# Kernel tuning notes

Measured on AMD Instinct MI355X. Metric: run time of the kernel, lower is better.

The kernel has to match this reference:

```python
import jax, jax.numpy as jnp
import numpy as np

EPS = 1e-5
NEG_SLOPE = 0.01  # F.leaky_relu default

N0, N1, N2 = 100000, 25000, 5000
E0, E1 = 800000, 160000
D_IN, D_HID, D_OUT = 256, 256, 128


def setup_inputs() -> dict:
    key = jax.random.key(0)
    ks = jax.random.split(key, 16)
    inp = {
        "x": jax.random.normal(ks[0], (N0, D_IN), dtype=jnp.float32),
        "src0": jax.random.randint(ks[1], (E0,), 0, N0, dtype=jnp.int32),
        "dst0": jax.random.randint(ks[2], (E0,), 0, N1, dtype=jnp.int32),
        "val0": jnp.arange(E0, dtype=jnp.int32),
        "src1": jax.random.randint(ks[3], (E1,), 0, N1, dtype=jnp.int32),
        "dst1": jax.random.randint(ks[4], (E1,), 0, N2, dtype=jnp.int32),
        "val1": jnp.arange(E1, dtype=jnp.int32),
        "timestamps": jax.random.randint(ks[5], (E0 + E1,), 0, 100, dtype=jnp.int32),
        "time": 50,
        "interval": 10,
        # SAGEConv layer 1 (in -> hidden): lin_l (bias) on aggregated, lin_r (no bias) on root
        "W1l": jax.random.normal(ks[6], (D_IN, D_HID), dtype=jnp.float32) / np.sqrt(D_IN),
        "W1r": jax.random.normal(ks[7], (D_IN, D_HID), dtype=jnp.float32) / np.sqrt(D_IN),
        "b1": jnp.zeros((D_HID,), dtype=jnp.float32),
        # BatchNorm1d params (eval mode: running stats)
        "g1": jnp.ones((D_HID,), dtype=jnp.float32),
        "bt1": jnp.zeros((D_HID,), dtype=jnp.float32),
        "rm1": jax.random.normal(ks[8], (D_HID,), dtype=jnp.float32) * 0.1,
        "rv1": jax.random.uniform(ks[9], (D_HID,), dtype=jnp.float32) + 0.5,
        # SAGEConv layer 2 (hidden -> out)
        "W2l": jax.random.normal(ks[10], (D_HID, D_OUT), dtype=jnp.float32) / np.sqrt(D_HID),
        "W2r": jax.random.normal(ks[11], (D_HID, D_OUT), dtype=jnp.float32) / np.sqrt(D_HID),
        "b2": jnp.zeros((D_OUT,), dtype=jnp.float32),
    }
    return inp


def _time_mask(val, timestamps, time, interval):
    # time_sparse keeps edges whose timestamp is in {time, ..., time+interval-1}
    ts = timestamps[val]
    return (ts >= time) & (ts < time + interval)


def _sage_conv(x_src, x_tgt, src, dst, mask, Wl, Wr, b, n_tgt):
    m = mask.astype(x_src.dtype)
    msg = x_src[src] * m[:, None]               # [E, D] gather + mask
    agg = jax.ops.segment_sum(msg, dst, num_segments=n_tgt)
    deg = jax.ops.segment_sum(m, dst, num_segments=n_tgt)
    agg = agg / jnp.maximum(deg, 1.0)[:, None]  # mean aggregation
    return agg @ Wl + b + x_tgt @ Wr


def reference(x, src0, dst0, val0, src1, dst1, val1, timestamps, time, interval,
              W1l, W1r, b1, g1, bt1, rm1, rv1, W2l, W2r, b2):
    # layer 0: N0 -> N1
    mask0 = _time_mask(val0, timestamps, time, interval)
    h = _sage_conv(x, x[:N1], src0, dst0, mask0, W1l, W1r, b1, N1)
    # BatchNorm1d (eval) + leaky_relu; dropout is identity in eval
    h = (h - rm1) * jax.lax.rsqrt(rv1 + EPS) * g1 + bt1
    h = jnp.where(h >= 0, h, NEG_SLOPE * h)
    # layer 1: N1 -> N2
    mask1 = _time_mask(val1, timestamps, time, interval)
    out = _sage_conv(h, h[:N2], src1, dst1, mask1, W2l, W2r, b2, N2)
    return out, mask1
```

## Files before the change

kernel.cpp:

```cpp
#include <hip/hip_runtime.h>

#define N1c 25000
#define N2c 5000
#define Dc 256
#define DOUTc 128
#define EPSc 1e-5f
#define NEGc 0.01f
#define CAPc 32

typedef __attribute__((ext_vector_type(8))) short short8;
typedef __attribute__((ext_vector_type(4))) float f32x4;

__device__ __forceinline__ ushort f2bf(float f) {
    unsigned u = __float_as_uint(f);
    u += 0x7fffu + ((u >> 16) & 1u);
    return (ushort)(u >> 16);
}
__device__ __forceinline__ float bf2f(ushort u) {
    return __uint_as_float(((unsigned)u) << 16);
}
__device__ __forceinline__ int imin(int a, int b) { return a < b ? a : b; }
__device__ __forceinline__ int imax(int a, int b) { return a > b ? a : b; }

__global__ __launch_bounds__(256) void prep_fill(
    const int* __restrict__ src0, const int* __restrict__ dst0, const int* __restrict__ val0,
    const int* __restrict__ src1, const int* __restrict__ dst1, const int* __restrict__ val1,
    const int* __restrict__ ts, const int* __restrict__ time_p, const int* __restrict__ itv_p,
    const float* __restrict__ W1l, const float* __restrict__ W1r,
    const float* __restrict__ W2l, const float* __restrict__ W2r,
    int E0, int E1,
    ushort* __restrict__ Bt1, ushort* __restrict__ Bt2,
    int* __restrict__ cnt0, int* __restrict__ cnt1,
    int* __restrict__ eidx0, int* __restrict__ eidx1,
    float* __restrict__ mask_out) {
    const int flat = blockIdx.x * blockDim.x + threadIdx.x;
    const int NT = gridDim.x * blockDim.x;
    const int t0 = *time_p, iv = *itv_p;

    for (int i = flat; i < 256 * 512; i += NT) {
        int n = i >> 9, k = i & 511;
        float v = (k < 256) ? W1l[(size_t)k * 256 + n] : W1r[(size_t)(k - 256) * 256 + n];
        Bt1[i] = f2bf(v);
    }
    for (int i = flat; i < 128 * 512; i += NT) {
        int n = i >> 9, k = i & 511;
        float v = (k < 256) ? W2l[(size_t)k * 128 + n] : W2r[(size_t)(k - 256) * 128 + n];
        Bt2[i] = f2bf(v);
    }
    for (int e = flat; e < E0; e += NT) {
        int t = ts[val0[e]];
        if (t >= t0 && t < t0 + iv) {
            int d = dst0[e];
            int pos = atomicAdd(&cnt0[d], 1);
            if (pos < CAPc) eidx0[d * CAPc + pos] = src0[e];
        }
    }
    for (int e = flat; e < E1; e += NT) {
        int t = ts[val1[e]];
        bool m = (t >= t0 && t < t0 + iv);
        mask_out[e] = m ? 1.0f : 0.0f;
        if (m) {
            int d = dst1[e];
            int pos = atomicAdd(&cnt1[d], 1);
            if (pos < CAPc) eidx1[d * CAPc + pos] = src1[e];
        }
    }
}

template <int VARIANT, int BMT, int NJW>
__global__ __launch_bounds__(512) void fused_gemm(
    const void* __restrict__ Asrc,
    const int* __restrict__ cnt, const int* __restrict__ eidx,
    const int* __restrict__ src, const int* __restrict__ dst,
    const int* __restrict__ val, const int* __restrict__ ts,
    const int* __restrict__ time_p, const int* __restrict__ itv_p, int E,
    const ushort* __restrict__ Bt,
    const float* __restrict__ bias,
    const float* __restrict__ g, const float* __restrict__ bt,
    const float* __restrict__ rm, const float* __restrict__ rv,
    void* __restrict__ Cout, int M) {
    constexpr int RT = BMT / 16;
    constexpr int RPW = BMT / 8;
    __shared__ ushort As[BMT][536];
    const int tid = threadIdx.x;
    const int wave = tid >> 6, lane = tid & 63;
    const int quad = lane >> 4, l16 = lane & 15;
    const int m0 = blockIdx.x * BMT;
    const float* Xf = (const float*)Asrc;
    const ushort* Hb = (const ushort*)Asrc;

    int ms_[RPW], cs_[RPW], my_[RPW];
#pragma unroll
    for (int i = 0; i < RPW; ++i) {
        ms_[i] = m0 + wave * RPW + i;
        cs_[i] = (ms_[i] < M) ? cnt[ms_[i]] : 0;
    }
#pragma unroll
    for (int i = 0; i < RPW; ++i)
        my_[i] = (ms_[i] < M && lane < CAPc) ? eidx[ms_[i] * CAPc + lane] : 0;
    float4 rtf_[RPW];
    ushort4 rtb_[RPW];
#pragma unroll
    for (int i = 0; i < RPW; ++i) {
        int mm = imax(0, imin(ms_[i], M - 1));
        if (VARIANT == 0) rtf_[i] = *(const float4*)(Xf + (size_t)mm * Dc + lane * 4);
        else              rtb_[i] = *(const ushort4*)(Hb + (size_t)mm * Dc + lane * 4);
    }
#pragma unroll
    for (int i = 0; i < RPW; ++i)
        my_[i] = (lane < cs_[i]) ? my_[i] : 0;

    float4 acc_[RPW];
#pragma unroll
    for (int i = 0; i < RPW; ++i) acc_[i] = make_float4(0.f, 0.f, 0.f, 0.f);

#pragma unroll
    for (int p = 0; p < RPW; p += 2) {
        float4 vf[2][4];
        ushort4 vb[2][4];
        int ccs[2];
#pragma unroll
        for (int q = 0; q < 2; ++q) {
            int cc = imin(cs_[p + q], CAPc);
            ccs[q] = cc;
#pragma unroll
            for (int u = 0; u < 4; ++u) {
                int e = imax(0, imin(u, cc - 1));
                int s = __shfl(my_[p + q], e, 64);
                if (VARIANT == 0) vf[q][u] = *(const float4*)(Xf + (size_t)s * Dc + lane * 4);
                else              vb[q][u] = *(const ushort4*)(Hb + (size_t)s * Dc + lane * 4);
            }
        }
#pragma unroll
        for (int q = 0; q < 2; ++q) {
            int i = p + q;
            int cc = ccs[q];
#pragma unroll
            for (int u = 0; u < 4; ++u) {
                if (u < cc) {
                    if (VARIANT == 0) {
                        acc_[i].x += vf[q][u].x; acc_[i].y += vf[q][u].y;
                        acc_[i].z += vf[q][u].z; acc_[i].w += vf[q][u].w;
                    } else {
                        acc_[i].x += bf2f(vb[q][u].x); acc_[i].y += bf2f(vb[q][u].y);
                        acc_[i].z += bf2f(vb[q][u].z); acc_[i].w += bf2f(vb[q][u].w);
                    }
                }
            }
            for (int jb = 4; jb < cc; jb += 4) {
#pragma unroll
                for (int u = 0; u < 4; ++u) {
                    int e = imin(jb + u, cc - 1);
                    int s = __shfl(my_[i], e, 64);
                    if (jb + u < cc) {
                        if (VARIANT == 0) {
                            float4 v = *(const float4*)(Xf + (size_t)s * Dc + lane * 4);
                            acc_[i].x += v.x; acc_[i].y += v.y; acc_[i].z += v.z; acc_[i].w += v.w;
                        } else {
                            ushort4 v = *(const ushort4*)(Hb + (size_t)s * Dc + lane * 4);
                            acc_[i].x += bf2f(v.x); acc_[i].y += bf2f(v.y);
                            acc_[i].z += bf2f(v.z); acc_[i].w += bf2f(v.w);
                        }
                    }
                }
            }
        }
    }
#pragma unroll
    for (int i = 0; i < RPW; ++i) {
        if (cs_[i] > CAPc) {
            float4 a = make_float4(0.f, 0.f, 0.f, 0.f);
            int t0 = *time_p, iv = *itv_p;
            for (int e = 0; e < E; ++e) {
                if (dst[e] != ms_[i]) continue;
                int t = ts[val[e]];
                if (t >= t0 && t < t0 + iv) {
                    if (VARIANT == 0) {
                        float4 v = *(const float4*)(Xf + (size_t)src[e] * Dc + lane * 4);
                        a.x += v.x; a.y += v.y; a.z += v.z; a.w += v.w;
                    } else {
                        ushort4 v = *(const ushort4*)(Hb + (size_t)src[e] * Dc + lane * 4);
                        a.x += bf2f(v.x); a.y += bf2f(v.y); a.z += bf2f(v.z); a.w += bf2f(v.w);
                    }
                }
            }
            acc_[i] = a;
        }
    }
#pragma unroll
    for (int i = 0; i < RPW; ++i) {
        int r = wave * RPW + i;
        if (ms_[i] >= M) {
            *(ushort4*)&As[r][lane * 4] = make_ushort4(0, 0, 0, 0);
            *(ushort4*)&As[r][256 + lane * 4] = make_ushort4(0, 0, 0, 0);
            continue;
        }
        float inv = 1.0f / fmaxf((float)cs_[i], 1.0f);
        ushort4 o;
        o.x = f2bf(acc_[i].x * inv); o.y = f2bf(acc_[i].y * inv);
        o.z = f2bf(acc_[i].z * inv); o.w = f2bf(acc_[i].w * inv);
        *(ushort4*)&As[r][lane * 4] = o;
        if (VARIANT == 0) {
            ushort4 ro;
            ro.x = f2bf(rtf_[i].x); ro.y = f2bf(rtf_[i].y);
            ro.z = f2bf(rtf_[i].z); ro.w = f2bf(rtf_[i].w);
            *(ushort4*)&As[r][256 + lane * 4] = ro;
        } else {
            *(ushort4*)&As[r][256 + lane * 4] = rtb_[i];
        }
    }
    __syncthreads();

    f32x4 acc[RT][NJW] = {};
    const ushort* Bw = Bt + (size_t)((wave * NJW) * 16 + l16) * 512 + quad * 8;
    for (int k0 = 0; k0 < 512; k0 += 32) {
        short8 af[RT];
#pragma unroll
        for (int rt = 0; rt < RT; ++rt)
            af[rt] = *(const short8*)&As[rt * 16 + l16][k0 + quad * 8];
        uint4 bfr[NJW];
#pragma unroll
        for (int jj = 0; jj < NJW; ++jj)
            bfr[jj] = *(const uint4*)(Bw + (size_t)jj * 16 * 512 + k0);
#pragma unroll
        for (int jj = 0; jj < NJW; ++jj) {
            short8 bf = *reinterpret_cast<const short8*>(&bfr[jj]);
#pragma unroll
            for (int rt = 0; rt < RT; ++rt)
                acc[rt][jj] = __builtin_amdgcn_mfma_f32_16x16x32_bf16(af[rt], bf, acc[rt][jj], 0, 0, 0);
        }
    }

#pragma unroll
    for (int jj = 0; jj < NJW; ++jj) {
        int gn = (wave * NJW + jj) * 16 + l16;
        float sc = 1.f, sh = bias[gn];
        if (VARIANT == 0) {
            float s = g[gn] * rsqrtf(rv[gn] + EPSc);
            sh = (bias[gn] - rm[gn]) * s + bt[gn];
            sc = s;
        }
#pragma unroll
        for (int rt = 0; rt < RT; ++rt) {
            int gmb = m0 + rt * 16 + quad * 4;
#pragma unroll
            for (int rr = 0; rr < 4; ++rr) {
                int gm = gmb + rr;
                if (gm >= M) continue;
                float v = acc[rt][jj][rr];
                if (VARIANT == 0) {
                    v = v * sc + sh;
                    v = v >= 0.f ? v : NEGc * v;
                    ((ushort*)Cout)[(size_t)gm * Dc + gn] = f2bf(v);
                } else {
                    ((float*)Cout)[(size_t)gm * DOUTc + gn] = v + sh;
                }
            }
        }
    }
}

extern "C" void kernel_launch(void* const* d_in, const int* in_sizes, int n_in,
                              void* d_out, int out_size, void* d_ws, size_t ws_size,
                              hipStream_t stream) {
    const float* x    = (const float*)d_in[0];
    const int* src0   = (const int*)d_in[1];
    const int* dst0   = (const int*)d_in[2];
    const int* val0   = (const int*)d_in[3];
    const int* src1   = (const int*)d_in[4];
    const int* dst1   = (const int*)d_in[5];
    const int* val1   = (const int*)d_in[6];
    const int* ts     = (const int*)d_in[7];
    const int* time_p = (const int*)d_in[8];
    const int* itv_p  = (const int*)d_in[9];
    const float* W1l  = (const float*)d_in[10];
    const float* W1r  = (const float*)d_in[11];
    const float* b1   = (const float*)d_in[12];
    const float* g1   = (const float*)d_in[13];
    const float* bt1  = (const float*)d_in[14];
    const float* rm1  = (const float*)d_in[15];
    const float* rv1  = (const float*)d_in[16];
    const float* W2l  = (const float*)d_in[17];
    const float* W2r  = (const float*)d_in[18];
    const float* b2   = (const float*)d_in[19];
    int E0 = in_sizes[1];
    int E1 = in_sizes[4];
    float* out = (float*)d_out;

    ushort* h    = (ushort*)d_ws;
    ushort* Bt1  = h    + (size_t)N1c * Dc;
    ushort* Bt2  = Bt1  + 256 * 512;
    int* ip      = (int*)(Bt2 + 128 * 512);
    int* cnt0    = ip;             ip += N1c;
    int* cnt1    = ip;             ip += N2c;
    int* eidx0   = ip;             ip += N1c * CAPc;
    int* eidx1   = ip;             ip += N2c * CAPc;
    float* mask_tail = out + (size_t)N2c * DOUTc;

    hipMemsetAsync(cnt0, 0, (size_t)(N1c + N2c) * sizeof(int), stream);

    prep_fill<<<2048, 256, 0, stream>>>(
        src0, dst0, val0, src1, dst1, val1, ts, time_p, itv_p,
        W1l, W1r, W2l, W2r, E0, E1, Bt1, Bt2,
        cnt0, cnt1, eidx0, eidx1, mask_tail);
    fused_gemm<0, 32, 2><<<(N1c + 31) / 32, 512, 0, stream>>>(
        x, cnt0, eidx0, src0, dst0, val0, ts, time_p, itv_p, E0,
        Bt1, b1, g1, bt1, rm1, rv1, h, N1c);
    fused_gemm<1, 16, 1><<<(N2c + 15) / 16, 512, 0, stream>>>(
        h, cnt1, eidx1, src1, dst1, val1, ts, time_p, itv_p, E1,
        Bt2, b2, nullptr, nullptr, nullptr, nullptr, out, N2c);
}
```

Measured before the change: 248.9 us.

## Pre-convert node features to bf16 and widen gather unroll

```diff
diff --git a/kernel.cpp b/kernel.cpp
--- a/kernel.cpp
+++ b/kernel.cpp
@@ -1,5 +1,6 @@
 #include <hip/hip_runtime.h>
 
+#define N0c 100000
 #define N1c 25000
 #define N2c 5000
 #define Dc 256
@@ -19,16 +20,21 @@
 __device__ __forceinline__ float bf2f(ushort u) {
     return __uint_as_float(((unsigned)u) << 16);
 }
+__device__ __forceinline__ unsigned pack2f(float lo, float hi) {
+    return ((unsigned)f2bf(lo)) | (((unsigned)f2bf(hi)) << 16);
+}
 __device__ __forceinline__ int imin(int a, int b) { return a < b ? a : b; }
 __device__ __forceinline__ int imax(int a, int b) { return a > b ? a : b; }
 
 __global__ __launch_bounds__(256) void prep_fill(
+    const float* __restrict__ x,
     const int* __restrict__ src0, const int* __restrict__ dst0, const int* __restrict__ val0,
     const int* __restrict__ src1, const int* __restrict__ dst1, const int* __restrict__ val1,
     const int* __restrict__ ts, const int* __restrict__ time_p, const int* __restrict__ itv_p,
     const float* __restrict__ W1l, const float* __restrict__ W1r,
     const float* __restrict__ W2l, const float* __restrict__ W2r,
     int E0, int E1,
+    ushort* __restrict__ xb,
     ushort* __restrict__ Bt1, ushort* __restrict__ Bt2,
     int* __restrict__ cnt0, int* __restrict__ cnt1,
     int* __restrict__ eidx0, int* __restrict__ eidx1,
@@ -37,6 +43,14 @@
     const int NT = gridDim.x * blockDim.x;
     const int t0 = *time_p, iv = *itv_p;
 
+    for (int i = flat; i < N0c * Dc / 8; i += NT) {
+        const float4 f0 = *(const float4*)(x + (size_t)i * 8);
+        const float4 f1 = *(const float4*)(x + (size_t)i * 8 + 4);
+        uint4 o;
+        o.x = pack2f(f0.x, f0.y); o.y = pack2f(f0.z, f0.w);
+        o.z = pack2f(f1.x, f1.y); o.w = pack2f(f1.z, f1.w);
+        *(uint4*)(xb + (size_t)i * 8) = o;
+    }
     for (int i = flat; i < 256 * 512; i += NT) {
         int n = i >> 9, k = i & 511;
         float v = (k < 256) ? W1l[(size_t)k * 256 + n] : W1r[(size_t)(k - 256) * 256 + n];
@@ -68,8 +82,8 @@
 }
 
 template <int VARIANT, int BMT, int NJW>
-__global__ __launch_bounds__(512) void fused_gemm(
-    const void* __restrict__ Asrc,
+__global__ __launch_bounds__(512, 4) void fused_gemm(
+    const ushort* __restrict__ Ab,
     const int* __restrict__ cnt, const int* __restrict__ eidx,
     const int* __restrict__ src, const int* __restrict__ dst,
     const int* __restrict__ val, const int* __restrict__ ts,
@@ -86,8 +100,6 @@
     const int wave = tid >> 6, lane = tid & 63;
     const int quad = lane >> 4, l16 = lane & 15;
     const int m0 = blockIdx.x * BMT;
-    const float* Xf = (const float*)Asrc;
-    const ushort* Hb = (const ushort*)Asrc;
 
     int ms_[RPW], cs_[RPW], my_[RPW];
 #pragma unroll
@@ -98,13 +110,11 @@
 #pragma unroll
     for (int i = 0; i < RPW; ++i)
         my_[i] = (ms_[i] < M && lane < CAPc) ? eidx[ms_[i] * CAPc + lane] : 0;
-    float4 rtf_[RPW];
     ushort4 rtb_[RPW];
 #pragma unroll
     for (int i = 0; i < RPW; ++i) {
         int mm = imax(0, imin(ms_[i], M - 1));
-        if (VARIANT == 0) rtf_[i] = *(const float4*)(Xf + (size_t)mm * Dc + lane * 4);
-        else              rtb_[i] = *(const ushort4*)(Hb + (size_t)mm * Dc + lane * 4);
+        rtb_[i] = *(const ushort4*)(Ab + (size_t)mm * Dc + lane * 4);
     }
 #pragma unroll
     for (int i = 0; i < RPW; ++i)
@@ -116,19 +126,17 @@
 
 #pragma unroll
     for (int p = 0; p < RPW; p += 2) {
-        float4 vf[2][4];
-        ushort4 vb[2][4];
+        ushort4 vb[2][8];
         int ccs[2];
 #pragma unroll
         for (int q = 0; q < 2; ++q) {
             int cc = imin(cs_[p + q], CAPc);
             ccs[q] = cc;
 #pragma unroll
-            for (int u = 0; u < 4; ++u) {
+            for (int u = 0; u < 8; ++u) {
                 int e = imax(0, imin(u, cc - 1));
                 int s = __shfl(my_[p + q], e, 64);
-                if (VARIANT == 0) vf[q][u] = *(const float4*)(Xf + (size_t)s * Dc + lane * 4);
-                else              vb[q][u] = *(const ushort4*)(Hb + (size_t)s * Dc + lane * 4);
+                vb[q][u] = *(const ushort4*)(Ab + (size_t)s * Dc + lane * 4);
             }
         }
 #pragma unroll
@@ -136,31 +144,21 @@
             int i = p + q;
             int cc = ccs[q];
 #pragma unroll
-            for (int u = 0; u < 4; ++u) {
+            for (int u = 0; u < 8; ++u) {
                 if (u < cc) {
-                    if (VARIANT == 0) {
-                        acc_[i].x += vf[q][u].x; acc_[i].y += vf[q][u].y;
-                        acc_[i].z += vf[q][u].z; acc_[i].w += vf[q][u].w;
-                    } else {
-                        acc_[i].x += bf2f(vb[q][u].x); acc_[i].y += bf2f(vb[q][u].y);
-                        acc_[i].z += bf2f(vb[q][u].z); acc_[i].w += bf2f(vb[q][u].w);
-                    }
-                }
-            }
-            for (int jb = 4; jb < cc; jb += 4) {
-#pragma unroll
-                for (int u = 0; u < 4; ++u) {
+                    acc_[i].x += bf2f(vb[q][u].x); acc_[i].y += bf2f(vb[q][u].y);
+                    acc_[i].z += bf2f(vb[q][u].z); acc_[i].w += bf2f(vb[q][u].w);
+                }
+            }
+            for (int jb = 8; jb < cc; jb += 8) {
+#pragma unroll
+                for (int u = 0; u < 8; ++u) {
                     int e = imin(jb + u, cc - 1);
                     int s = __shfl(my_[i], e, 64);
                     if (jb + u < cc) {
-                        if (VARIANT == 0) {
-                            float4 v = *(const float4*)(Xf + (size_t)s * Dc + lane * 4);
-                            acc_[i].x += v.x; acc_[i].y += v.y; acc_[i].z += v.z; acc_[i].w += v.w;
-                        } else {
-                            ushort4 v = *(const ushort4*)(Hb + (size_t)s * Dc + lane * 4);
-                            acc_[i].x += bf2f(v.x); acc_[i].y += bf2f(v.y);
-                            acc_[i].z += bf2f(v.z); acc_[i].w += bf2f(v.w);
-                        }
+                        ushort4 v = *(const ushort4*)(Ab + (size_t)s * Dc + lane * 4);
+                        acc_[i].x += bf2f(v.x); acc_[i].y += bf2f(v.y);
+                        acc_[i].z += bf2f(v.z); acc_[i].w += bf2f(v.w);
                     }
                 }
             }
@@ -175,13 +173,8 @@
                 if (dst[e] != ms_[i]) continue;
                 int t = ts[val[e]];
                 if (t >= t0 && t < t0 + iv) {
-                    if (VARIANT == 0) {
-                        float4 v = *(const float4*)(Xf + (size_t)src[e] * Dc + lane * 4);
-                        a.x += v.x; a.y += v.y; a.z += v.z; a.w += v.w;
-                    } else {
-                        ushort4 v = *(const ushort4*)(Hb + (size_t)src[e] * Dc + lane * 4);
-                        a.x += bf2f(v.x); a.y += bf2f(v.y); a.z += bf2f(v.z); a.w += bf2f(v.w);
-                    }
+                    ushort4 v = *(const ushort4*)(Ab + (size_t)src[e] * Dc + lane * 4);
+                    a.x += bf2f(v.x); a.y += bf2f(v.y); a.z += bf2f(v.z); a.w += bf2f(v.w);
                 }
             }
             acc_[i] = a;
@@ -200,14 +193,7 @@
         o.x = f2bf(acc_[i].x * inv); o.y = f2bf(acc_[i].y * inv);
         o.z = f2bf(acc_[i].z * inv); o.w = f2bf(acc_[i].w * inv);
         *(ushort4*)&As[r][lane * 4] = o;
-        if (VARIANT == 0) {
-            ushort4 ro;
-            ro.x = f2bf(rtf_[i].x); ro.y = f2bf(rtf_[i].y);
-            ro.z = f2bf(rtf_[i].z); ro.w = f2bf(rtf_[i].w);
-            *(ushort4*)&As[r][256 + lane * 4] = ro;
-        } else {
-            *(ushort4*)&As[r][256 + lane * 4] = rtb_[i];
-        }
+        *(ushort4*)&As[r][256 + lane * 4] = rtb_[i];
     }
     __syncthreads();
 
@@ -287,7 +273,8 @@
     int E1 = in_sizes[4];
     float* out = (float*)d_out;
 
-    ushort* h    = (ushort*)d_ws;
+    ushort* xb   = (ushort*)d_ws;
+    ushort* h    = xb   + (size_t)N0c * Dc;
     ushort* Bt1  = h    + (size_t)N1c * Dc;
     ushort* Bt2  = Bt1  + 256 * 512;
     int* ip      = (int*)(Bt2 + 128 * 512);
@@ -300,11 +287,11 @@
     hipMemsetAsync(cnt0, 0, (size_t)(N1c + N2c) * sizeof(int), stream);
 
     prep_fill<<<2048, 256, 0, stream>>>(
-        src0, dst0, val0, src1, dst1, val1, ts, time_p, itv_p,
-        W1l, W1r, W2l, W2r, E0, E1, Bt1, Bt2,
+        x, src0, dst0, val0, src1, dst1, val1, ts, time_p, itv_p,
+        W1l, W1r, W2l, W2r, E0, E1, xb, Bt1, Bt2,
         cnt0, cnt1, eidx0, eidx1, mask_tail);
     fused_gemm<0, 32, 2><<<(N1c + 31) / 32, 512, 0, stream>>>(
-        x, cnt0, eidx0, src0, dst0, val0, ts, time_p, itv_p, E0,
+        xb, cnt0, eidx0, src0, dst0, val0, ts, time_p, itv_p, E0,
         Bt1, b1, g1, bt1, rm1, rv1, h, N1c);
     fused_gemm<1, 16, 1><<<(N2c + 15) / 16, 512, 0, stream>>>(
         h, cnt1, eidx1, src1, dst1, val1, ts, time_p, itv_p, E1,
```

Result: slower. 264.1 us (+6.1%).
